# Kernel tuning notes

Hardware: AMD Instinct MI355X
Metric: run time of the kernel (lower is better)

Reference implementation:

```python
import jax, jax.numpy as jnp
from jax import lax
import numpy as np

VOCAB, L, D, K = 50000, 8921, 300, 10
B, T = 8, 2048


def setup_inputs() -> dict:
    key = jax.random.key(0)
    k_ids, k_e, k_cw, k_cb, k_u = jax.random.split(key, 5)
    ids = jax.random.randint(k_ids, (B, T), 0, VOCAB, dtype=jnp.int32)
    embed_w = jax.random.normal(k_e, (VOCAB, D), dtype=jnp.float32) * 0.02
    embed_w = embed_w.at[0].set(0.0)  # padding_idx=0
    conv_w = jax.random.normal(k_cw, (D, D, K), dtype=jnp.float32) * 0.02  # (out, in, k) == torch OIH
    conv_b = jax.random.normal(k_cb, (D,), dtype=jnp.float32) * 0.02
    U = jax.random.normal(k_u, (L, D), dtype=jnp.float32)
    fc_bias = jnp.zeros((L,), dtype=jnp.float32)
    return {"ids": ids, "embed_w": embed_w, "conv_w": conv_w, "conv_b": conv_b, "U": U, "fc_bias": fc_bias}


def reference(ids, embed_w, conv_w, conv_b, U, fc_bias):
    # Embedding lookup (padding_idx row already zeroed in table)
    e = embed_w[ids]                       # (B, T, D)
    x = jnp.transpose(e, (0, 2, 1))        # (B, D, T)
    pad = conv_w.shape[-1] - 1             # torch padding=filter_size-1 (both sides)
    h = lax.conv_general_dilated(
        x, conv_w, window_strides=(1,), padding=[(pad, pad)],
        dimension_numbers=("NCH", "OIH", "NCH"))
    h = jax.nn.relu(h + conv_b[None, :, None])   # (B, D, T') where T' = T + K - 1
    attn = jax.nn.softmax(jnp.einsum("ld,bdt->blt", U, h), axis=-1)  # (B, L, T')
    z = jnp.einsum("blt,bdt->bld", attn, h)                          # (B, L, D)
    logits = jnp.einsum("bld,ld->bl", z, U) + fc_bias                # (B, L)
    return logits
```

## Files before the change

### kernel.cpp

```cpp
#include <hip/hip_runtime.h>

#define VOCAB   50000
#define LDIM    8921
#define DDIM    300
#define DPAD    320
#define KSZ     10
#define BATCH   8
#define TSEQ    2048
#define PADL    9
#define TPRIME  2057
#define TPADDED 2066
#define LPAD    8928

#define TSTG    32
#define NTT     65
#define TALLOC  (NTT * TSTG)
#define LBLK    70

typedef short s8v __attribute__((ext_vector_type(8)));
typedef float f4v __attribute__((ext_vector_type(4)));

typedef const __attribute__((address_space(1))) unsigned int* gas_ptr;
typedef __attribute__((address_space(3))) unsigned int* las_ptr;

__device__ inline unsigned short f2bf(float f) {
  union { float f; unsigned u; } v; v.f = f;
  unsigned r = v.u + 0x7FFF + ((v.u >> 16) & 1);
  return (unsigned short)(r >> 16);
}

__global__ __launch_bounds__(256) void prep_kernel(
    const float* __restrict__ w, const float* __restrict__ U,
    unsigned short* __restrict__ wT, unsigned short* __restrict__ Ub) {
  int bid = blockIdx.x;
  if (bid < KSZ * DPAD) {
    int k = bid / DPAD, o = bid % DPAD;
    for (int i = threadIdx.x; i < DPAD; i += 256) {
      float v = (o < DDIM && i < DDIM) ? w[((size_t)o * DDIM + i) * KSZ + k] : 0.0f;
      wT[((size_t)k * DPAD + o) * DPAD + i] = f2bf(v);
    }
  } else {
    int l = bid - KSZ * DPAD;
    for (int d = threadIdx.x; d < DPAD; d += 256) {
      float v = (l < LDIM && d < DDIM) ? U[(size_t)l * DDIM + d] : 0.0f;
      Ub[(size_t)l * DPAD + d] = f2bf(v);
    }
  }
}

#define CTN 80
#define CROWS 89
#define CSTRIDE 328
__global__ __launch_bounds__(256) void conv_mfma_kernel(
    const int* __restrict__ ids, const float* __restrict__ embed_w,
    const unsigned short* __restrict__ wT,
    const float* __restrict__ bias, unsigned short* __restrict__ h) {
  __shared__ unsigned short xls[CROWS * CSTRIDE];
  int b = blockIdx.x & 7, tb = blockIdx.x >> 3;
  int t0 = tb * CTN;
  int tid = threadIdx.x;
  {
    const int* idsb = ids + b * TSEQ;
    for (int idx = tid; idx < CROWS * 40; idx += 256) {
      int rr = idx / 40, c8 = idx % 40;
      int tau = t0 + rr;
      bool inr = (tau >= PADL) && (tau < PADL + TSEQ);
      unsigned short pk[8];
      if (inr) {
        int row = idsb[tau - PADL];
        const float* src = embed_w + (size_t)row * DDIM + c8 * 8;
        float4 lo = (c8 * 8 + 3 < DDIM) ? *(const float4*)&src[0] : make_float4(0, 0, 0, 0);
        float4 hi = (c8 * 8 + 7 < DDIM) ? *(const float4*)&src[4] : make_float4(0, 0, 0, 0);
        pk[0] = f2bf(lo.x); pk[1] = f2bf(lo.y); pk[2] = f2bf(lo.z); pk[3] = f2bf(lo.w);
        pk[4] = f2bf(hi.x); pk[5] = f2bf(hi.y); pk[6] = f2bf(hi.z); pk[7] = f2bf(hi.w);
      } else {
#pragma unroll
        for (int e = 0; e < 8; ++e) pk[e] = 0;
      }
      *(int4*)&xls[rr * CSTRIDE + c8 * 8] = *(const int4*)pk;
    }
  }
  __syncthreads();
  int w = tid >> 6, lane = tid & 63;
  int l15 = lane & 15, quad = lane >> 4;
  int ob = w * 80;
  f4v acc[5][5];
#pragma unroll
  for (int mf = 0; mf < 5; ++mf) {
    float bv[4];
#pragma unroll
    for (int rr = 0; rr < 4; ++rr) {
      int o = ob + mf * 16 + quad * 4 + rr;
      bv[rr] = (o < DDIM) ? bias[o] : 0.0f;
    }
#pragma unroll
    for (int nf = 0; nf < 5; ++nf) {
      acc[mf][nf][0] = bv[0]; acc[mf][nf][1] = bv[1];
      acc[mf][nf][2] = bv[2]; acc[mf][nf][3] = bv[3];
    }
  }
  const unsigned short* wl = wT + (size_t)(ob + l15) * DPAD + quad * 8;
  s8v Aping[5], Apong[5];
#pragma unroll
  for (int mf = 0; mf < 5; ++mf) Aping[mf] = *(const s8v*)&wl[mf * 16 * DPAD];
#pragma unroll
  for (int mf = 0; mf < 5; ++mf) Apong[mf] = *(const s8v*)&wl[mf * 16 * DPAD + 32];
  for (int ii = 0; ii < 100; ii += 2) {
    {
      int kc = ii / 10, it = ii % 10;
      s8v Bv[5];
#pragma unroll
      for (int nf = 0; nf < 5; ++nf)
        Bv[nf] = *(const s8v*)&xls[(nf * 16 + l15 + kc) * CSTRIDE + it * 32 + quad * 8];
#pragma unroll
      for (int mf = 0; mf < 5; ++mf)
#pragma unroll
        for (int nf = 0; nf < 5; ++nf)
          acc[mf][nf] = __builtin_amdgcn_mfma_f32_16x16x32_bf16(Aping[mf], Bv[nf], acc[mf][nf], 0, 0, 0);
      int p = ii + 2;
      if (p < 100) {
        int kp = p / 10, itp = p % 10;
        const unsigned short* wp = wl + (size_t)kp * (DPAD * DPAD) + itp * 32;
#pragma unroll
        for (int mf = 0; mf < 5; ++mf) Aping[mf] = *(const s8v*)&wp[mf * 16 * DPAD];
      }
    }
    {
      int kc = (ii + 1) / 10, it = (ii + 1) % 10;
      s8v Bv[5];
#pragma unroll
      for (int nf = 0; nf < 5; ++nf)
        Bv[nf] = *(const s8v*)&xls[(nf * 16 + l15 + kc) * CSTRIDE + it * 32 + quad * 8];
#pragma unroll
      for (int mf = 0; mf < 5; ++mf)
#pragma unroll
        for (int nf = 0; nf < 5; ++nf)
          acc[mf][nf] = __builtin_amdgcn_mfma_f32_16x16x32_bf16(Apong[mf], Bv[nf], acc[mf][nf], 0, 0, 0);
      int p = ii + 3;
      if (p < 100) {
        int kp = p / 10, itp = p % 10;
        const unsigned short* wp = wl + (size_t)kp * (DPAD * DPAD) + itp * 32;
#pragma unroll
        for (int mf = 0; mf < 5; ++mf) Apong[mf] = *(const s8v*)&wp[mf * 16 * DPAD];
      }
    }
  }
#pragma unroll
  for (int mf = 0; mf < 5; ++mf) {
    int obase = ob + mf * 16 + quad * 4;
#pragma unroll
    for (int nf = 0; nf < 5; ++nf) {
      int t = t0 + nf * 16 + l15;
      bool live = t < TPRIME;
      unsigned short pk[4];
#pragma unroll
      for (int rr = 0; rr < 4; ++rr)
        pk[rr] = live ? f2bf(fmaxf(acc[mf][nf][rr], 0.0f)) : (unsigned short)0;
      *(uint2*)&h[((size_t)b * TALLOC + t) * DPAD + obase] = *(uint2*)pk;
    }
  }
}

__global__ __launch_bounds__(256) void attn_mfma_kernel(
    const unsigned short* __restrict__ h, const unsigned short* __restrict__ Ub,
    const float* __restrict__ fcb, float* __restrict__ out) {
  __shared__ unsigned short hls[3 * TSTG * DPAD];
  int b = blockIdx.x & 7, lb = blockIdx.x >> 3;
  int tid = threadIdx.x;
  int w = tid >> 6, lane = tid & 63;
  int l15 = lane & 15, quad = lane >> 4;
  const unsigned short* hb = h + (size_t)b * TALLOC * DPAD;

  s8v A[2][10];
  {
    int lr0 = lb * 128 + w * 32 + l15;
#pragma unroll
    for (int mf = 0; mf < 2; ++mf) {
      int lr = lr0 + mf * 16;
      if (lr >= LPAD) lr = LPAD - 1;
      const unsigned short* up = Ub + (size_t)lr * DPAD + quad * 8;
#pragma unroll
      for (int kc = 0; kc < 10; ++kc)
        A[mf][kc] = *(const s8v*)&up[kc * 32];
    }
  }
  asm volatile("s_waitcnt vmcnt(0)" ::: "memory");

  int srcoff[5];
#pragma unroll
  for (int j = 0; j < 5; ++j) {
    int g = w * 320 + j * 64 + lane;
    int r = g / 40, c = g % 40;
    srcoff[j] = r * DPAD + ((c ^ (r & 7)) * 8);
  }

  int phase = lb % NTT;
  int tp0 = phase;
  int tp1 = (phase + 1 < NTT) ? phase + 1 : phase + 1 - NTT;

#pragma unroll
  for (int j = 0; j < 5; ++j)
    __builtin_amdgcn_global_load_lds(
        (gas_ptr)(const void*)(hb + (size_t)tp0 * (TSTG * DPAD) + srcoff[j]),
        (las_ptr)(void*)&hls[w * 2560 + j * 512], 16, 0, 0);
#pragma unroll
  for (int j = 0; j < 5; ++j)
    __builtin_amdgcn_global_load_lds(
        (gas_ptr)(const void*)(hb + (size_t)tp1 * (TSTG * DPAD) + srcoff[j]),
        (las_ptr)(void*)&hls[10240 + w * 2560 + j * 512], 16, 0, 0);
  asm volatile("s_waitcnt vmcnt(5)" ::: "memory");
  __builtin_amdgcn_s_barrier();

  float se[2][4], sw[2][4];
#pragma unroll
  for (int mf = 0; mf < 2; ++mf)
#pragma unroll
    for (int r = 0; r < 4; ++r) { se[mf][r] = 0.0f; sw[mf][r] = 0.0f; }

  int xr8 = (l15 & 7) * 8;
  int rowb0 = l15 * DPAD;
  int rowb1 = (16 + l15) * DPAD;
  int cur = 0, d2 = 2;
  int tp2 = (phase + 2 < NTT) ? phase + 2 : phase + 2 - NTT;
  const f4v vzero = {0.0f, 0.0f, 0.0f, 0.0f};

  for (int t = 0; t < NTT; ++t) {
    if (t + 2 < NTT) {
      const unsigned short* src = hb + (size_t)tp2 * (TSTG * DPAD);
      int dstb = d2 * 10240 + w * 2560;
#pragma unroll
      for (int j = 0; j < 5; ++j)
        __builtin_amdgcn_global_load_lds((gas_ptr)(const void*)(src + srcoff[j]),
                                         (las_ptr)(void*)&hls[dstb + j * 512],
                                         16, 0, 0);
      tp2 = (tp2 + 1 < NTT) ? tp2 + 1 : 0;
    }
    const unsigned short* bufc = &hls[cur * 10240];
    f4v a00, a01, a10, a11;
    __builtin_amdgcn_s_setprio(1);
    {
      int ko = (quad * 8) ^ xr8;
      s8v Bv0 = *(const s8v*)&bufc[rowb0 + ko];
      s8v Bv1 = *(const s8v*)&bufc[rowb1 + ko];
      a00 = __builtin_amdgcn_mfma_f32_16x16x32_bf16(A[0][0], Bv0, vzero, 0, 0, 0);
      a01 = __builtin_amdgcn_mfma_f32_16x16x32_bf16(A[0][0], Bv1, vzero, 0, 0, 0);
      a10 = __builtin_amdgcn_mfma_f32_16x16x32_bf16(A[1][0], Bv0, vzero, 0, 0, 0);
      a11 = __builtin_amdgcn_mfma_f32_16x16x32_bf16(A[1][0], Bv1, vzero, 0, 0, 0);
    }
#pragma unroll
    for (int kc = 1; kc < 10; ++kc) {
      int ko = (kc * 32 + quad * 8) ^ xr8;
      s8v Bv0 = *(const s8v*)&bufc[rowb0 + ko];
      s8v Bv1 = *(const s8v*)&bufc[rowb1 + ko];
      a00 = __builtin_amdgcn_mfma_f32_16x16x32_bf16(A[0][kc], Bv0, a00, 0, 0, 0);
      a01 = __builtin_amdgcn_mfma_f32_16x16x32_bf16(A[0][kc], Bv1, a01, 0, 0, 0);
      a10 = __builtin_amdgcn_mfma_f32_16x16x32_bf16(A[1][kc], Bv0, a10, 0, 0, 0);
      a11 = __builtin_amdgcn_mfma_f32_16x16x32_bf16(A[1][kc], Bv1, a11, 0, 0, 0);
    }
    __builtin_amdgcn_s_setprio(0);
#pragma unroll
    for (int r = 0; r < 4; ++r) {
      float s0 = a00[r], s1 = a01[r];
      float e0 = __expf(s0), e1 = __expf(s1);
      se[0][r] += e0 + e1;
      sw[0][r] = fmaf(e0, s0, sw[0][r]);
      sw[0][r] = fmaf(e1, s1, sw[0][r]);
      float s2 = a10[r], s3 = a11[r];
      float e2 = __expf(s2), e3 = __expf(s3);
      se[1][r] += e2 + e3;
      sw[1][r] = fmaf(e2, s2, sw[1][r]);
      sw[1][r] = fmaf(e3, s3, sw[1][r]);
    }
    if (t + 2 < NTT) {
      asm volatile("s_waitcnt vmcnt(5)" ::: "memory");
    } else {
      asm volatile("s_waitcnt vmcnt(0)" ::: "memory");
    }
    __builtin_amdgcn_s_barrier();
    cur = (cur + 1 < 3) ? cur + 1 : 0;
    d2 = (d2 + 1 < 3) ? d2 + 1 : 0;
  }

#pragma unroll
  for (int mf = 0; mf < 2; ++mf)
#pragma unroll
    for (int r = 0; r < 4; ++r) {
      float a = se[mf][r], c = sw[mf][r];
#pragma unroll
      for (int off = 1; off < 16; off <<= 1) {
        a += __shfl_xor(a, off, 64);
        c += __shfl_xor(c, off, 64);
      }
      if (l15 == 0) {
        int l = lb * 128 + w * 32 + mf * 16 + quad * 4 + r;
        if (l < LDIM) out[(size_t)b * LDIM + l] = c / (a - 23.0f) + fcb[l];
      }
    }
}

extern "C" void kernel_launch(void* const* d_in, const int* in_sizes, int n_in,
                              void* d_out, int out_size, void* d_ws, size_t ws_size,
                              hipStream_t stream) {
  const int*   ids     = (const int*)d_in[0];
  const float* embed_w = (const float*)d_in[1];
  const float* conv_w  = (const float*)d_in[2];
  const float* conv_b  = (const float*)d_in[3];
  const float* U       = (const float*)d_in[4];
  const float* fc_bias = (const float*)d_in[5];
  float* out = (float*)d_out;

  unsigned char* p = (unsigned char*)d_ws;
  unsigned short* hb = (unsigned short*)p;                 p += (size_t)BATCH * TALLOC * DPAD * 2;
  unsigned short* wT = (unsigned short*)p;                 p += (size_t)KSZ * DPAD * DPAD * 2;
  unsigned short* Ub = (unsigned short*)p;

  hipLaunchKernelGGL(prep_kernel, dim3(KSZ * DPAD + LPAD), dim3(256), 0, stream,
                     conv_w, U, wT, Ub);
  hipLaunchKernelGGL(conv_mfma_kernel, dim3(BATCH * 26), dim3(256), 0, stream,
                     ids, embed_w, wT, conv_b, hb);
  hipLaunchKernelGGL(attn_mfma_kernel, dim3(BATCH * LBLK), dim3(256), 0, stream,
                     hb, Ub, fc_bias, out);
}
```

Baseline: 312.3 us.

## Switch attention kernel to double-buffered LDS pipeline with sequential tile order

```diff
diff --git a/kernel.cpp b/kernel.cpp
--- a/kernel.cpp
+++ b/kernel.cpp
@@ -161,10 +161,10 @@
   }
 }
 
-__global__ __launch_bounds__(256) void attn_mfma_kernel(
+__global__ __launch_bounds__(256, 3) void attn_mfma_kernel(
     const unsigned short* __restrict__ h, const unsigned short* __restrict__ Ub,
     const float* __restrict__ fcb, float* __restrict__ out) {
-  __shared__ unsigned short hls[3 * TSTG * DPAD];
+  __shared__ unsigned short hls[2 * TSTG * DPAD];
   int b = blockIdx.x & 7, lb = blockIdx.x >> 3;
   int tid = threadIdx.x;
   int w = tid >> 6, lane = tid & 63;
@@ -184,7 +184,6 @@
         A[mf][kc] = *(const s8v*)&up[kc * 32];
     }
   }
-  asm volatile("s_waitcnt vmcnt(0)" ::: "memory");
 
   int srcoff[5];
 #pragma unroll
@@ -194,21 +193,12 @@
     srcoff[j] = r * DPAD + ((c ^ (r & 7)) * 8);
   }
 
-  int phase = lb % NTT;
-  int tp0 = phase;
-  int tp1 = (phase + 1 < NTT) ? phase + 1 : phase + 1 - NTT;
-
 #pragma unroll
   for (int j = 0; j < 5; ++j)
-    __builtin_amdgcn_global_load_lds(
-        (gas_ptr)(const void*)(hb + (size_t)tp0 * (TSTG * DPAD) + srcoff[j]),
-        (las_ptr)(void*)&hls[w * 2560 + j * 512], 16, 0, 0);
-#pragma unroll
-  for (int j = 0; j < 5; ++j)
-    __builtin_amdgcn_global_load_lds(
-        (gas_ptr)(const void*)(hb + (size_t)tp1 * (TSTG * DPAD) + srcoff[j]),
-        (las_ptr)(void*)&hls[10240 + w * 2560 + j * 512], 16, 0, 0);
-  asm volatile("s_waitcnt vmcnt(5)" ::: "memory");
+    __builtin_amdgcn_global_load_lds((gas_ptr)(const void*)(hb + srcoff[j]),
+                                     (las_ptr)(void*)&hls[w * 2560 + j * 512],
+                                     16, 0, 0);
+  asm volatile("s_waitcnt vmcnt(0)" ::: "memory");
   __builtin_amdgcn_s_barrier();
 
   float se[2][4], sw[2][4];
@@ -220,22 +210,19 @@
   int xr8 = (l15 & 7) * 8;
   int rowb0 = l15 * DPAD;
   int rowb1 = (16 + l15) * DPAD;
-  int cur = 0, d2 = 2;
-  int tp2 = (phase + 2 < NTT) ? phase + 2 : phase + 2 - NTT;
+  int bufsel = 0;
   const f4v vzero = {0.0f, 0.0f, 0.0f, 0.0f};
-
   for (int t = 0; t < NTT; ++t) {
-    if (t + 2 < NTT) {
-      const unsigned short* src = hb + (size_t)tp2 * (TSTG * DPAD);
-      int dstb = d2 * 10240 + w * 2560;
+    if (t + 1 < NTT) {
+      const unsigned short* src = hb + (size_t)(t + 1) * TSTG * DPAD;
+      int dstb = (bufsel ^ 1) * 10240 + w * 2560;
 #pragma unroll
       for (int j = 0; j < 5; ++j)
         __builtin_amdgcn_global_load_lds((gas_ptr)(const void*)(src + srcoff[j]),
                                          (las_ptr)(void*)&hls[dstb + j * 512],
                                          16, 0, 0);
-      tp2 = (tp2 + 1 < NTT) ? tp2 + 1 : 0;
-    }
-    const unsigned short* bufc = &hls[cur * 10240];
+    }
+    const unsigned short* bufc = &hls[bufsel * 10240];
     f4v a00, a01, a10, a11;
     __builtin_amdgcn_s_setprio(1);
     {
@@ -271,14 +258,9 @@
       sw[1][r] = fmaf(e2, s2, sw[1][r]);
       sw[1][r] = fmaf(e3, s3, sw[1][r]);
     }
-    if (t + 2 < NTT) {
-      asm volatile("s_waitcnt vmcnt(5)" ::: "memory");
-    } else {
-      asm volatile("s_waitcnt vmcnt(0)" ::: "memory");
-    }
+    asm volatile("s_waitcnt vmcnt(0)" ::: "memory");
     __builtin_amdgcn_s_barrier();
-    cur = (cur + 1 < 3) ? cur + 1 : 0;
-    d2 = (d2 + 1 < 3) ? d2 + 1 : 0;
+    bufsel ^= 1;
   }
 
 #pragma unroll
```

New measurement: 283.8 us, median of 2. 9.1% less time.
